# Performance work log

Measured on AMD Instinct MI355X. Metric: run time of the kernel, lower is better.

Reference implementation:

```python
import jax, jax.numpy as jnp
import numpy as np

B, C, H, W = 16, 256, 32, 32
NH = 4
GROUPS = 8
EPS = 1e-5


def setup_inputs() -> dict:
    key = jax.random.key(0)
    ks = jax.random.split(key, 7)
    x = jax.random.normal(ks[0], (B, C, H, W), dtype=jnp.float32)
    norm_w = jnp.ones((C,), jnp.float32)
    norm_b = jnp.zeros((C,), jnp.float32)
    # 1x1 convs == per-pixel linear maps; store as [out, in] matrices
    qkv_w = jax.random.normal(ks[1], (3 * C, C), dtype=jnp.float32) * (1.0 / np.sqrt(C))
    qkv_b = jnp.zeros((3 * C,), jnp.float32)
    proj_w = jax.random.normal(ks[2], (C, C), dtype=jnp.float32) * (1.0 / np.sqrt(C))
    proj_b = jnp.zeros((C,), jnp.float32)
    return {"x": x, "norm_w": norm_w, "norm_b": norm_b,
            "qkv_w": qkv_w, "qkv_b": qkv_b, "proj_w": proj_w, "proj_b": proj_b}


def _group_norm(x, w, b):
    # x: [B, C, H, W], GROUPS groups over channel dim
    b_, c, h, w_ = x.shape
    xg = x.reshape(b_, GROUPS, c // GROUPS, h, w_)
    mean = xg.mean(axis=(2, 3, 4), keepdims=True)
    var = xg.var(axis=(2, 3, 4), keepdims=True)
    xg = (xg - mean) * jax.lax.rsqrt(var + EPS)
    x = xg.reshape(b_, c, h, w_)
    return x * w[None, :, None, None] + b[None, :, None, None]


def reference(x, norm_w, norm_b, qkv_w, qkv_b, proj_w, proj_b):
    b, c, h, w = x.shape
    nh, d = NH, c // NH
    s = h * w
    hn = _group_norm(x, norm_w, norm_b)
    # 1x1 conv: [3C, C] x [B, C, S] -> [B, 3C, S]
    hf = hn.reshape(b, c, s)
    qkv = jnp.einsum('oc,bcs->bos', qkv_w, hf) + qkv_b[None, :, None]
    # channel layout: (t h d); -> [B, 3, nh, d, S] -> per-tensor [B, nh, S, d]
    qkv = qkv.reshape(b, 3, nh, d, s)
    q = jnp.transpose(qkv[:, 0], (0, 1, 3, 2))  # [B, nh, S, d]
    k = jnp.transpose(qkv[:, 1], (0, 1, 3, 2))
    v = jnp.transpose(qkv[:, 2], (0, 1, 3, 2))
    scale = 1.0 / np.sqrt(d).astype(np.float32)
    attn = jnp.einsum('bhqd,bhkd->bhqk', q, k) * scale
    attn = jax.nn.softmax(attn, axis=-1)
    out = jnp.einsum('bhqk,bhkd->bhqd', attn, v)        # [B, nh, S, d]
    out = jnp.transpose(out, (0, 1, 3, 2)).reshape(b, c, s)  # b (h d) s
    out = jnp.einsum('oc,bcs->bos', proj_w, out) + proj_b[None, :, None]
    return x + out.reshape(b, c, h, w)
```

## Files before the change

### kernel.cpp

```cpp
#include <hip/hip_runtime.h>

#define NB 16
#define NC 256
#define NS 1024
#define NNH 4
#define ND 64
#define GN_EPS 1e-5f

typedef __attribute__((ext_vector_type(8))) short short8;
typedef __attribute__((ext_vector_type(4))) float f32x4;

static __device__ __forceinline__ ushort f2bf(float x) {
  union { float f; unsigned u; } c; c.f = x;
  unsigned r = (c.u + 0x7fffu + ((c.u >> 16) & 1u)) >> 16;
  return (ushort)r;
}
static __device__ __forceinline__ unsigned cvt_pk_bf16(float lo, float hi) {
  unsigned r;
  asm("v_cvt_pk_bf16_f32 %0, %1, %2" : "=v"(r) : "v"(lo), "v"(hi));
  return r;
}

__global__ __launch_bounds__(256) void gnstat_wconv_kernel(
    const float* __restrict__ x, float2* __restrict__ partials,
    const float* __restrict__ qw, const float* __restrict__ pw,
    ushort* __restrict__ wbf) {
  const int bid = blockIdx.x;
  const int t = threadIdx.x;
  if (bid >= 1024) {
    const int i = (bid - 1024) * 256 + t;
    const float4 v = (i < 49152) ? *(const float4*)(qw + (size_t)i * 4)
                                 : *(const float4*)(pw + (size_t)(i - 49152) * 4);
    ushort4 u;
    u.x = f2bf(v.x); u.y = f2bf(v.y); u.z = f2bf(v.z); u.w = f2bf(v.w);
    *(ushort4*)(wbf + (size_t)i * 4) = u;
    return;
  }
  const int bg = bid >> 3, part = bid & 7;
  const float4* xv = (const float4*)(x + (size_t)bg * 32768 + part * 4096);
  float s1 = 0.f, s2 = 0.f;
  #pragma unroll
  for (int i = 0; i < 4; ++i) {
    float4 v = xv[t + 256 * i];
    s1 += v.x + v.y + v.z + v.w;
    s2 += v.x * v.x + v.y * v.y + v.z * v.z + v.w * v.w;
  }
  #pragma unroll
  for (int o = 32; o > 0; o >>= 1) {
    s1 += __shfl_down(s1, o, 64);
    s2 += __shfl_down(s2, o, 64);
  }
  __shared__ float rs1[4], rs2[4];
  const int wid = t >> 6;
  if ((t & 63) == 0) { rs1[wid] = s1; rs2[wid] = s2; }
  __syncthreads();
  if (t == 0) {
    partials[bid] = make_float2(rs1[0] + rs1[1] + rs1[2] + rs1[3],
                                rs2[0] + rs2[1] + rs2[2] + rs2[3]);
  }
}

__global__ __launch_bounds__(256) void gnapply_kernel(
    const float* __restrict__ x, const float* __restrict__ nw,
    const float* __restrict__ nb, const float2* __restrict__ partials,
    ushort* __restrict__ hnT) {
  const int bid = blockIdx.x;
  const int bg = bid >> 3, st = bid & 7;
  const int b = bg >> 3, gg = bg & 7;
  const int t = threadIdx.x;

  float s1 = 0.f, s2 = 0.f;
  #pragma unroll
  for (int j = 0; j < 8; ++j) {
    const float2 p = partials[bg * 8 + j];
    s1 += p.x; s2 += p.y;
  }
  const float mean = s1 * (1.f / 32768.f);
  const float var = s2 * (1.f / 32768.f) - mean * mean;
  const float rstd = rsqrtf(var + GN_EPS);

  __shared__ ushort tile[128][36];
  const int s4 = (t & 31) * 4;
  #pragma unroll
  for (int i = 0; i < 4; ++i) {
    const int c = (t >> 5) + 8 * i;
    const int cg = gg * 32 + c;
    const float wgt = nw[cg] * rstd;
    const float bia = nb[cg] - mean * wgt;
    const float4 v = *(const float4*)(x + ((size_t)(b * NC + cg)) * NS +
                                      st * 128 + s4);
    tile[s4 + 0][c] = f2bf(v.x * wgt + bia);
    tile[s4 + 1][c] = f2bf(v.y * wgt + bia);
    tile[s4 + 2][c] = f2bf(v.z * wgt + bia);
    tile[s4 + 3][c] = f2bf(v.w * wgt + bia);
  }
  __syncthreads();
  #pragma unroll
  for (int i = 0; i < 4; ++i) {
    const int idx = t + 256 * i;
    const int sr = idx >> 3, ch4 = (idx & 7) * 4;
    const ushort4 u = *(const ushort4*)&tile[sr][ch4];
    *(ushort4*)(hnT + ((size_t)(b * NS + st * 128 + sr)) * NC + gg * 32 + ch4) = u;
  }
}

template <int EPI, int YDIM>
__global__ __launch_bounds__(256) void mfma_gemm_kernel(
    const ushort* __restrict__ Wbf, const float* __restrict__ bias,
    const ushort* __restrict__ DATA, const float* __restrict__ X,
    ushort* __restrict__ qT, ushort* __restrict__ kT, ushort* __restrict__ vN,
    float* __restrict__ OUT) {
  __shared__ char smem[32768];
  char* T1 = smem;
  char* T2 = smem + 16384;
  const int nwg = 8 * YDIM * NB;
  const int o_id = blockIdx.x;
  const int wg = (o_id & 7) * (nwg >> 3) + (o_id >> 3);
  const int b = wg / (8 * YDIM);
  const int o0 = ((wg >> 3) % YDIM) * 128, s0 = (wg & 7) * 128;
  const int t = threadIdx.x, w = t >> 6, l = t & 63;
  const int g = l >> 4, li = l & 15;
  const ushort* wrow = Wbf + (size_t)o0 * NC;
  const ushort* drow = DATA + ((size_t)b * NS + s0) * NC;

  f32x4 acc[4][4];
  #pragma unroll
  for (int i = 0; i < 4; ++i)
    #pragma unroll
    for (int j = 0; j < 4; ++j) acc[i][j] = (f32x4){0.f, 0.f, 0.f, 0.f};

  const int oh = (w >> 1) * 64, sh = (w & 1) * 64;
  const int srow = t >> 3, sce = (t & 7) * 8;
  const int sds = srow * 128 + (((t & 7) * 16) ^ ((srow & 7) << 4));

  short8 r1[4], r2[4];
  #pragma unroll
  for (int i = 0; i < 4; ++i) {
    r1[i] = *(const short8*)(wrow + (size_t)(srow + 32 * i) * NC + sce);
    r2[i] = *(const short8*)(drow + (size_t)(srow + 32 * i) * NC + sce);
  }

  for (int k0 = 0; k0 < NC; k0 += 64) {
    __syncthreads();
    #pragma unroll
    for (int i = 0; i < 4; ++i) {
      *(short8*)(T1 + sds + i * 4096) = r1[i];
      *(short8*)(T2 + sds + i * 4096) = r2[i];
    }
    __syncthreads();
    if (k0 + 64 < NC) {
      #pragma unroll
      for (int i = 0; i < 4; ++i) {
        r1[i] = *(const short8*)(wrow + (size_t)(srow + 32 * i) * NC + k0 + 64 + sce);
        r2[i] = *(const short8*)(drow + (size_t)(srow + 32 * i) * NC + k0 + 64 + sce);
      }
    }
    __builtin_amdgcn_s_setprio(1);
    #pragma unroll
    for (int kk = 0; kk < 2; ++kk) {
      short8 af[4], bfr[4];
      #pragma unroll
      for (int ms = 0; ms < 4; ++ms) {
        const int row = oh + ms * 16 + li;
        af[ms] = *(const short8*)(T1 + row * 128 +
                                  ((kk * 64 + g * 16) ^ ((row & 7) << 4)));
      }
      #pragma unroll
      for (int ns = 0; ns < 4; ++ns) {
        const int row = sh + ns * 16 + li;
        bfr[ns] = *(const short8*)(T2 + row * 128 +
                                   ((kk * 64 + g * 16) ^ ((row & 7) << 4)));
      }
      #pragma unroll
      for (int ms = 0; ms < 4; ++ms)
        #pragma unroll
        for (int ns = 0; ns < 4; ++ns)
          acc[ms][ns] = __builtin_amdgcn_mfma_f32_16x16x32_bf16(
              af[ms], bfr[ns], acc[ms][ns], 0, 0, 0);
    }
    __builtin_amdgcn_s_setprio(0);
  }

  const int ob = o0 + oh;
  if (EPI == 0) {
    const int tsr = ob >> 8;
    const int h = (ob >> 6) & 3;
    if (tsr < 2) {
      const float sc = (tsr == 0) ? 0.18033688f : 1.0f;
      ushort* dst = (tsr == 0 ? qT : kT) + ((size_t)(b * 4 + h)) * NS * ND;
      #pragma unroll
      for (int ms = 0; ms < 4; ++ms) {
        const float4 bv = *(const float4*)(bias + ob + ms * 16 + g * 4);
        const int d0 = ms * 16 + g * 4;
        #pragma unroll
        for (int ns = 0; ns < 4; ++ns) {
          const int s = s0 + sh + ns * 16 + li;
          ushort4 pk;
          pk.x = f2bf((acc[ms][ns][0] + bv.x) * sc);
          pk.y = f2bf((acc[ms][ns][1] + bv.y) * sc);
          pk.z = f2bf((acc[ms][ns][2] + bv.z) * sc);
          pk.w = f2bf((acc[ms][ns][3] + bv.w) * sc);
          *(ushort4*)(dst + (size_t)s * ND + d0) = pk;
        }
      }
    } else {
      ushort* dst = vN + ((size_t)(b * 4 + h)) * ND * NS;
      #pragma unroll
      for (int ms = 0; ms < 4; ++ms) {
        const float4 bv = *(const float4*)(bias + ob + ms * 16 + g * 4);
        const float bvr[4] = {bv.x, bv.y, bv.z, bv.w};
        #pragma unroll
        for (int r = 0; r < 4; ++r) {
          const int d = ms * 16 + g * 4 + r;
          #pragma unroll
          for (int ns = 0; ns < 4; ++ns) {
            const int s = s0 + sh + ns * 16 + li;
            dst[(size_t)d * NS + s] = f2bf(acc[ms][ns][r] + bvr[r]);
          }
        }
      }
    }
  } else {
    float* outb = OUT + (size_t)b * NC * NS;
    const float* xb = X + (size_t)b * NC * NS;
    #pragma unroll
    for (int ms = 0; ms < 4; ++ms) {
      const float4 bv = *(const float4*)(bias + ob + ms * 16 + g * 4);
      const float bvr[4] = {bv.x, bv.y, bv.z, bv.w};
      #pragma unroll
      for (int r = 0; r < 4; ++r) {
        const int c = ob + ms * 16 + g * 4 + r;
        #pragma unroll
        for (int ns = 0; ns < 4; ++ns) {
          const int s = s0 + sh + ns * 16 + li;
          const size_t a = (size_t)c * NS + s;
          outb[a] = acc[ms][ns][r] + bvr[r] + xb[a];
        }
      }
    }
  }
}

__global__ __launch_bounds__(512, 2) void attn_kernel(
    const ushort* __restrict__ qT, const ushort* __restrict__ kT,
    const ushort* __restrict__ vN, ushort* __restrict__ att2) {
  __shared__ char smem[65536];
  const int o_id = blockIdx.x;
  const int wg = (o_id & 7) * 32 + (o_id >> 3);
  const int b = wg >> 4, h = (wg >> 2) & 3;
  const int sq0 = (wg & 3) * 256;
  const int t = threadIdx.x, w = t >> 6, l = t & 63;
  const int g = l >> 4, li = l & 15;
  const int sw = (li & 7) << 4;
  char* Ps = smem + 32768 + w * 4096;
  const size_t bh = (size_t)(b * 4 + h);
  const ushort* qbase = qT + bh * NS * ND + (size_t)sq0 * ND;
  const ushort* kbase = kT + bh * NS * ND;
  const ushort* vbase = vN + bh * ND * NS;

  #pragma unroll
  for (int i = 0; i < 4; ++i) {
    const int f = t + 512 * i;
    const int row = f >> 3, c8 = f & 7;
    short8 v = *(const short8*)(qbase + (size_t)row * ND + c8 * 8);
    *(short8*)(smem + 32768 + ((row * 128 + c8 * 16) ^ ((row & 7) << 4))) = v;
  }
  __syncthreads();
  short8 aq[2][2];
  #pragma unroll
  for (int m = 0; m < 2; ++m) {
    const int row = w * 32 + m * 16 + li;
    aq[m][0] = *(const short8*)(smem + 32768 + row * 128 + ((g * 16) ^ sw));
    aq[m][1] = *(const short8*)(smem + 32768 + row * 128 + ((64 + g * 16) ^ sw));
  }

  const int srow = t >> 3, sc8 = t & 7;
  const int sdst = srow * 128 + ((sc8 * 16) ^ ((srow & 7) << 4));
  {
    short8 k0 = *(const short8*)(kbase + (size_t)srow * ND + sc8 * 8);
    short8 v0 = *(const short8*)(vbase + (size_t)srow * NS + sc8 * 8);
    *(short8*)(smem + sdst) = k0;
    *(short8*)(smem + 8192 + sdst) = v0;
  }

  f32x4 acc[2][4];
  #pragma unroll
  for (int m = 0; m < 2; ++m)
    #pragma unroll
    for (int dt = 0; dt < 4; ++dt) acc[m][dt] = (f32x4){0.f, 0.f, 0.f, 0.f};
  float lsum[2] = {0.f, 0.f};

  for (int kt = 0; kt < 16; ++kt) {
    __syncthreads();
    char* Kc = smem + (kt & 1) * 16384;
    char* Vc = Kc + 8192;

    short8 nk, nv;
    if (kt < 15) {
      nk = *(const short8*)(kbase + (size_t)(kt + 1) * 64 * ND +
                            (size_t)srow * ND + sc8 * 8);
      nv = *(const short8*)(vbase + (size_t)srow * NS + (kt + 1) * 64 + sc8 * 8);
    }

    __builtin_amdgcn_s_setprio(1);
    #pragma unroll
    for (int kst = 0; kst < 4; ++kst) {
      const int krow = kst * 16 + li;
      const short8 bk0 = *(const short8*)(Kc + krow * 128 + ((g * 16) ^ sw));
      const short8 bk1 = *(const short8*)(Kc + krow * 128 + ((64 + g * 16) ^ sw));
      #pragma unroll
      for (int m = 0; m < 2; ++m) {
        f32x4 sT = {0.f, 0.f, 0.f, 0.f};
        sT = __builtin_amdgcn_mfma_f32_16x16x32_bf16(bk0, aq[m][0], sT, 0, 0, 0);
        sT = __builtin_amdgcn_mfma_f32_16x16x32_bf16(bk1, aq[m][1], sT, 0, 0, 0);
        const float p0 = __builtin_amdgcn_exp2f(sT[0]);
        const float p1 = __builtin_amdgcn_exp2f(sT[1]);
        const float p2 = __builtin_amdgcn_exp2f(sT[2]);
        const float p3 = __builtin_amdgcn_exp2f(sT[3]);
        lsum[m] += (p0 + p1) + (p2 + p3);
        uint2 pk;
        pk.x = cvt_pk_bf16(p0, p1);
        pk.y = cvt_pk_bf16(p2, p3);
        *(uint2*)(Ps + (m * 16 + li) * 128 + ((kst * 32 + 8 * g) ^ sw)) = pk;
      }
    }
    __builtin_amdgcn_s_setprio(0);

    __builtin_amdgcn_s_setprio(1);
    #pragma unroll
    for (int ks2 = 0; ks2 < 2; ++ks2) {
      short8 pa[2];
      #pragma unroll
      for (int m = 0; m < 2; ++m)
        pa[m] = *(const short8*)(Ps + (m * 16 + li) * 128 +
                                 ((ks2 * 64 + g * 16) ^ sw));
      #pragma unroll
      for (int dt = 0; dt < 4; ++dt) {
        const int vrow = dt * 16 + li;
        const short8 bv = *(const short8*)(Vc + vrow * 128 +
                                           ((ks2 * 64 + g * 16) ^ sw));
        #pragma unroll
        for (int m = 0; m < 2; ++m)
          acc[m][dt] = __builtin_amdgcn_mfma_f32_16x16x32_bf16(
              pa[m], bv, acc[m][dt], 0, 0, 0);
      }
    }
    __builtin_amdgcn_s_setprio(0);

    if (kt < 15) {
      char* Kn = smem + ((kt + 1) & 1) * 16384;
      *(short8*)(Kn + sdst) = nk;
      *(short8*)(Kn + 8192 + sdst) = nv;
    }
  }

  float lr[2][4];
  #pragma unroll
  for (int m = 0; m < 2; ++m) {
    float s = lsum[m];
    s += __shfl_xor(s, 16, 64);
    s += __shfl_xor(s, 32, 64);
    const float linv = 1.f / s;
    #pragma unroll
    for (int r = 0; r < 4; ++r) lr[m][r] = __shfl(linv, g * 4 + r, 64);
  }

  ushort* obase = att2 + ((size_t)b * NS + sq0 + w * 32) * NC + h * 64;
  #pragma unroll
  for (int m = 0; m < 2; ++m)
    #pragma unroll
    for (int dt = 0; dt < 4; ++dt)
      #pragma unroll
      for (int r = 0; r < 4; ++r)
        obase[(size_t)(m * 16 + g * 4 + r) * NC + dt * 16 + li] =
            f2bf(acc[m][dt][r] * lr[m][r]);
}

extern "C" void kernel_launch(void* const* d_in, const int* in_sizes, int n_in,
                              void* d_out, int out_size, void* d_ws, size_t ws_size,
                              hipStream_t stream) {
  const float* x      = (const float*)d_in[0];
  const float* norm_w = (const float*)d_in[1];
  const float* norm_b = (const float*)d_in[2];
  const float* qkv_w  = (const float*)d_in[3];
  const float* qkv_b  = (const float*)d_in[4];
  const float* proj_w = (const float*)d_in[5];
  const float* proj_b = (const float*)d_in[6];
  float* out = (float*)d_out;

  ushort* hnT  = (ushort*)d_ws;
  ushort* qT   = hnT + (size_t)4194304;
  ushort* kT   = qT + (size_t)4194304;
  ushort* vN   = kT + (size_t)4194304;
  ushort* att2 = vN + (size_t)4194304;
  ushort* wbf  = att2 + (size_t)4194304;
  float2* partials = (float2*)(wbf + (size_t)262144);
  ushort* wq = wbf;
  ushort* wp = wbf + (size_t)196608;

  gnstat_wconv_kernel<<<dim3(1280), 256, 0, stream>>>(
      x, partials, qkv_w, proj_w, wbf);
  gnapply_kernel<<<dim3(1024), 256, 0, stream>>>(
      x, norm_w, norm_b, partials, hnT);
  mfma_gemm_kernel<0, 6><<<dim3(768), 256, 0, stream>>>(
      wq, qkv_b, hnT, nullptr, qT, kT, vN, nullptr);
  attn_kernel<<<dim3(256), 512, 0, stream>>>(qT, kT, vN, att2);
  mfma_gemm_kernel<1, 2><<<dim3(256), 256, 0, stream>>>(
      wp, proj_b, att2, x, nullptr, nullptr, nullptr, out);
}
```

Baseline: 60.95 us.

## Fuse GroupNorm apply into QKV GEMM prologue and transpose x during stats pass

The statistics kernel now also transposes x into a bf16 [B,S,C] buffer, and the separate GroupNorm-apply kernel is removed. The QKV GEMM computes per-channel scale and shift from the partial sums and applies them to the data tile while staging it into shared memory. This avoids one full read of x and one kernel launch, at the cost of extra ALU work in the GEMM load path. It also rounds x to bf16 before normalisation rather than after.

```diff
diff --git a/kernel.cpp b/kernel.cpp
--- a/kernel.cpp
+++ b/kernel.cpp
@@ -21,10 +21,10 @@
   return r;
 }
 
-__global__ __launch_bounds__(256) void gnstat_wconv_kernel(
-    const float* __restrict__ x, float2* __restrict__ partials,
-    const float* __restrict__ qw, const float* __restrict__ pw,
-    ushort* __restrict__ wbf) {
+__global__ __launch_bounds__(256) void gnstatT_wconv_kernel(
+    const float* __restrict__ x, ushort* __restrict__ xT,
+    float2* __restrict__ partials, const float* __restrict__ qw,
+    const float* __restrict__ pw, ushort* __restrict__ wbf) {
   const int bid = blockIdx.x;
   const int t = threadIdx.x;
   if (bid >= 1024) {
@@ -36,71 +36,42 @@
     *(ushort4*)(wbf + (size_t)i * 4) = u;
     return;
   }
-  const int bg = bid >> 3, part = bid & 7;
-  const float4* xv = (const float4*)(x + (size_t)bg * 32768 + part * 4096);
+  const int bg = bid >> 3, st = bid & 7;
+  const int b = bg >> 3, gg = bg & 7;
+
+  __shared__ ushort tile[128][36];
+  __shared__ float rs1[4], rs2[4];
+  const int s4 = (t & 31) * 4;
   float s1 = 0.f, s2 = 0.f;
   #pragma unroll
   for (int i = 0; i < 4; ++i) {
-    float4 v = xv[t + 256 * i];
+    const int c = (t >> 5) + 8 * i;
+    const int cg = gg * 32 + c;
+    const float4 v = *(const float4*)(x + ((size_t)(b * NC + cg)) * NS +
+                                      st * 128 + s4);
     s1 += v.x + v.y + v.z + v.w;
     s2 += v.x * v.x + v.y * v.y + v.z * v.z + v.w * v.w;
+    tile[s4 + 0][c] = f2bf(v.x);
+    tile[s4 + 1][c] = f2bf(v.y);
+    tile[s4 + 2][c] = f2bf(v.z);
+    tile[s4 + 3][c] = f2bf(v.w);
   }
   #pragma unroll
   for (int o = 32; o > 0; o >>= 1) {
     s1 += __shfl_down(s1, o, 64);
     s2 += __shfl_down(s2, o, 64);
   }
-  __shared__ float rs1[4], rs2[4];
-  const int wid = t >> 6;
-  if ((t & 63) == 0) { rs1[wid] = s1; rs2[wid] = s2; }
+  if ((t & 63) == 0) { rs1[t >> 6] = s1; rs2[t >> 6] = s2; }
   __syncthreads();
-  if (t == 0) {
+  if (t == 0)
     partials[bid] = make_float2(rs1[0] + rs1[1] + rs1[2] + rs1[3],
                                 rs2[0] + rs2[1] + rs2[2] + rs2[3]);
-  }
-}
-
-__global__ __launch_bounds__(256) void gnapply_kernel(
-    const float* __restrict__ x, const float* __restrict__ nw,
-    const float* __restrict__ nb, const float2* __restrict__ partials,
-    ushort* __restrict__ hnT) {
-  const int bid = blockIdx.x;
-  const int bg = bid >> 3, st = bid & 7;
-  const int b = bg >> 3, gg = bg & 7;
-  const int t = threadIdx.x;
-
-  float s1 = 0.f, s2 = 0.f;
-  #pragma unroll
-  for (int j = 0; j < 8; ++j) {
-    const float2 p = partials[bg * 8 + j];
-    s1 += p.x; s2 += p.y;
-  }
-  const float mean = s1 * (1.f / 32768.f);
-  const float var = s2 * (1.f / 32768.f) - mean * mean;
-  const float rstd = rsqrtf(var + GN_EPS);
-
-  __shared__ ushort tile[128][36];
-  const int s4 = (t & 31) * 4;
-  #pragma unroll
-  for (int i = 0; i < 4; ++i) {
-    const int c = (t >> 5) + 8 * i;
-    const int cg = gg * 32 + c;
-    const float wgt = nw[cg] * rstd;
-    const float bia = nb[cg] - mean * wgt;
-    const float4 v = *(const float4*)(x + ((size_t)(b * NC + cg)) * NS +
-                                      st * 128 + s4);
-    tile[s4 + 0][c] = f2bf(v.x * wgt + bia);
-    tile[s4 + 1][c] = f2bf(v.y * wgt + bia);
-    tile[s4 + 2][c] = f2bf(v.z * wgt + bia);
-    tile[s4 + 3][c] = f2bf(v.w * wgt + bia);
-  }
-  __syncthreads();
   #pragma unroll
   for (int i = 0; i < 4; ++i) {
     const int idx = t + 256 * i;
     const int sr = idx >> 3, ch4 = (idx & 7) * 4;
     const ushort4 u = *(const ushort4*)&tile[sr][ch4];
-    *(ushort4*)(hnT + ((size_t)(b * NS + st * 128 + sr)) * NC + gg * 32 + ch4) = u;
+    *(ushort4*)(xT + ((size_t)(b * NS + st * 128 + sr)) * NC + gg * 32 + ch4) = u;
   }
 }
 
@@ -108,9 +79,13 @@
 __global__ __launch_bounds__(256) void mfma_gemm_kernel(
     const ushort* __restrict__ Wbf, const float* __restrict__ bias,
     const ushort* __restrict__ DATA, const float* __restrict__ X,
+    const float* __restrict__ nw, const float* __restrict__ nb,
+    const float2* __restrict__ partials,
     ushort* __restrict__ qT, ushort* __restrict__ kT, ushort* __restrict__ vN,
     float* __restrict__ OUT) {
   __shared__ char smem[32768];
+  __shared__ float2 sm_wb[256];
+  __shared__ float2 sm_g[8];
   char* T1 = smem;
   char* T2 = smem + 16384;
   const int nwg = 8 * YDIM * NB;
@@ -123,12 +98,6 @@
   const ushort* wrow = Wbf + (size_t)o0 * NC;
   const ushort* drow = DATA + ((size_t)b * NS + s0) * NC;
 
-  f32x4 acc[4][4];
-  #pragma unroll
-  for (int i = 0; i < 4; ++i)
-    #pragma unroll
-    for (int j = 0; j < 4; ++j) acc[i][j] = (f32x4){0.f, 0.f, 0.f, 0.f};
-
   const int oh = (w >> 1) * 64, sh = (w & 1) * 64;
   const int srow = t >> 3, sce = (t & 7) * 8;
   const int sds = srow * 128 + (((t & 7) * 16) ^ ((srow & 7) << 4));
@@ -140,12 +109,56 @@
     r2[i] = *(const short8*)(drow + (size_t)(srow + 32 * i) * NC + sce);
   }
 
+  if (EPI == 0) {
+    if (t < 8) {
+      float s1 = 0.f, s2 = 0.f;
+      #pragma unroll
+      for (int j = 0; j < 8; ++j) {
+        const float2 p = partials[(b * 8 + t) * 8 + j];
+        s1 += p.x; s2 += p.y;
+      }
+      const float mean = s1 * (1.f / 32768.f);
+      const float var = s2 * (1.f / 32768.f) - mean * mean;
+      sm_g[t] = make_float2(mean, rsqrtf(var + GN_EPS));
+    }
+    __syncthreads();
+    const float2 ms = sm_g[t >> 5];
+    const float wgt = nw[t] * ms.y;
+    sm_wb[t] = make_float2(wgt, nb[t] - ms.x * wgt);
+  }
+
+  f32x4 acc[4][4];
+  #pragma unroll
+  for (int i = 0; i < 4; ++i)
+    #pragma unroll
+    for (int j = 0; j < 4; ++j) acc[i][j] = (f32x4){0.f, 0.f, 0.f, 0.f};
+
   for (int k0 = 0; k0 < NC; k0 += 64) {
     __syncthreads();
     #pragma unroll
-    for (int i = 0; i < 4; ++i) {
+    for (int i = 0; i < 4; ++i)
       *(short8*)(T1 + sds + i * 4096) = r1[i];
-      *(short8*)(T2 + sds + i * 4096) = r2[i];
+    if (EPI == 0) {
+      float2 wb[8];
+      #pragma unroll
+      for (int j = 0; j < 8; ++j) wb[j] = sm_wb[k0 + sce + j];
+      #pragma unroll
+      for (int i = 0; i < 4; ++i) {
+        union { short8 s; unsigned u[4]; } a, o;
+        a.s = r2[i];
+        #pragma unroll
+        for (int j = 0; j < 4; ++j) {
+          const float lo = __uint_as_float(a.u[j] << 16);
+          const float hi = __uint_as_float(a.u[j] & 0xffff0000u);
+          o.u[j] = cvt_pk_bf16(fmaf(lo, wb[2 * j].x, wb[2 * j].y),
+                               fmaf(hi, wb[2 * j + 1].x, wb[2 * j + 1].y));
+        }
+        *(short8*)(T2 + sds + i * 4096) = o.s;
+      }
+    } else {
+      #pragma unroll
+      for (int i = 0; i < 4; ++i)
+        *(short8*)(T2 + sds + i * 4096) = r2[i];
     }
     __syncthreads();
     if (k0 + 64 < NC) {
@@ -388,8 +401,8 @@
   const float* proj_b = (const float*)d_in[6];
   float* out = (float*)d_out;
 
-  ushort* hnT  = (ushort*)d_ws;
-  ushort* qT   = hnT + (size_t)4194304;
+  ushort* xT   = (ushort*)d_ws;
+  ushort* qT   = xT + (size_t)4194304;
   ushort* kT   = qT + (size_t)4194304;
   ushort* vN   = kT + (size_t)4194304;
   ushort* att2 = vN + (size_t)4194304;
@@ -398,13 +411,11 @@
   ushort* wq = wbf;
   ushort* wp = wbf + (size_t)196608;
 
-  gnstat_wconv_kernel<<<dim3(1280), 256, 0, stream>>>(
-      x, partials, qkv_w, proj_w, wbf);
-  gnapply_kernel<<<dim3(1024), 256, 0, stream>>>(
-      x, norm_w, norm_b, partials, hnT);
+  gnstatT_wconv_kernel<<<dim3(1280), 256, 0, stream>>>(
+      x, xT, partials, qkv_w, proj_w, wbf);
   mfma_gemm_kernel<0, 6><<<dim3(768), 256, 0, stream>>>(
-      wq, qkv_b, hnT, nullptr, qT, kT, vN, nullptr);
+      wq, qkv_b, xT, nullptr, norm_w, norm_b, partials, qT, kT, vN, nullptr);
   attn_kernel<<<dim3(256), 512, 0, stream>>>(qT, kT, vN, att2);
   mfma_gemm_kernel<1, 2><<<dim3(256), 256, 0, stream>>>(
-      wp, proj_b, att2, x, nullptr, nullptr, nullptr, out);
-}
+      wp, proj_b, att2, x, nullptr, nullptr, nullptr, nullptr, nullptr, nullptr, out);
+}
```

After: 58.47 us, median of 2. 1.04x faster.
